# Performance work log

Hardware: AMD Instinct MI355X
Metric: run time of the kernel (lower is better)

Reference implementation:

```python
import jax, jax.numpy as jnp
import numpy as np
import math


def setup_inputs() -> dict:
    key = jax.random.key(0)
    kq, kk, kv = jax.random.split(key, 3)
    B, H, S, D = 8, 12, 4096, 64
    q = jax.random.normal(kq, (B, H, S, D), dtype=jnp.float32)
    k = jax.random.normal(kk, (B, H, S, D), dtype=jnp.float32)
    v = jax.random.normal(kv, (B, H, S, D), dtype=jnp.float32)
    return {"q": q, "k": k, "v": v}


def reference(q, k, v):
    B, H, S, D = q.shape
    topk = int(2 * math.sqrt(S))  # 128 for S=4096
    # importance = mean + std (torch.std is unbiased -> ddof=1)
    importance = q.mean(axis=-1) + jnp.std(q, axis=-1, ddof=1)  # [B,H,S]
    _, idx = jax.lax.top_k(importance, topk)  # [B,H,topk]
    idx_e = idx[..., None]  # [B,H,topk,1]
    q_s = jnp.take_along_axis(q, idx_e, axis=2)  # [B,H,topk,D]
    k_s = jnp.take_along_axis(k, idx_e, axis=2)
    v_s = jnp.take_along_axis(v, idx_e, axis=2)
    scores = jnp.einsum('bhtd,bhsd->bhts', q_s, k_s) / math.sqrt(D)
    attn = jax.nn.softmax(scores, axis=-1)
    out_s = jnp.einsum('bhts,bhsd->bhtd', attn, v_s)  # [B,H,topk,D]
    # scatter back into a full tensor (torch uses empty_like; we use zeros
    # for the unselected positions so the output is deterministic)
    bI = jnp.arange(B)[:, None, None]
    hI = jnp.arange(H)[None, :, None]
    out = jnp.zeros_like(v).at[bI, hI, idx].set(out_s)  # [B,H,S,D]
    Himg = int(math.sqrt(S))
    return out.reshape(B, -1, Himg, Himg)  # [B, H*D, Himg, Himg]
```

## Files before the change

### kernel.cpp

```cpp
#include <hip/hip_runtime.h>
#include <hip/hip_fp16.h>
#include <math.h>

#define BH_N 96
#define S_N 4096
#define D_N 64
#define TOPK 128

typedef unsigned long long ull;

__device__ __forceinline__ ull orderKey(double d) {
  ull u = (ull)__double_as_longlong(d);
  if (u & 0x8000000000000000ULL) u = ~u;
  else u |= 0x8000000000000000ULL;
  return u;
}

__global__ __launch_bounds__(256)
void imp_zero_kernel(const float* __restrict__ q, float* __restrict__ out,
                     ull* __restrict__ keys) {
  const int tid = threadIdx.x;
  const size_t off = (size_t)blockIdx.x * 1024 + (size_t)tid * 4;
  const float4 v = *reinterpret_cast<const float4*>(q + off);
  float4 z; z.x = z.y = z.z = z.w = 0.f;
  *reinterpret_cast<float4*>(out + off) = z;

  double s  = (double)v.x + (double)v.y + (double)v.z + (double)v.w;
  double ss = (double)v.x * v.x + (double)v.y * v.y +
              (double)v.z * v.z + (double)v.w * v.w;
#pragma unroll
  for (int m = 1; m < 16; m <<= 1) {
    s  += __shfl_xor(s, m, 64);
    ss += __shfl_xor(ss, m, 64);
  }
  if ((tid & 15) == 0) {
    double mean = s * (1.0 / 64.0);
    double var = (ss - s * s * (1.0 / 64.0)) * (1.0 / 63.0);
    if (var < 0.0) var = 0.0;
    keys[(size_t)blockIdx.x * 16 + (tid >> 4)] = orderKey(mean + sqrt(var));
  }
}

__global__ __launch_bounds__(1024)
void sel_kernel(const ull* __restrict__ keys, int* __restrict__ idx_out) {
  __shared__ int red[2][16];
  __shared__ int s_idx[TOPK];
  __shared__ int s_tidx[1024];
  __shared__ int s_cnt, s_tcnt;

  const int tid = threadIdx.x;
  const int lane = tid & 63;
  const int wv = tid >> 6;
  const int bh = blockIdx.x;
  const ull* kb = keys + (size_t)bh * S_N;

  ull key[4];
#pragma unroll
  for (int i = 0; i < 4; ++i) key[i] = kb[i * 1024 + tid];

  if (tid == 0) { s_cnt = 0; s_tcnt = 0; }

  ull lo = 0ULL, hi = ~0ULL;
  int p = 0;
  while (lo < hi) {
    ull d = hi - lo;
    ull mid = lo + (d >> 1) + (d & 1ULL);
    int c = 0;
#pragma unroll
    for (int i = 0; i < 4; ++i) c += __popcll(__ballot(key[i] >= mid));
    if (lane == 0) red[p][wv] = c;
    __syncthreads();
    int total = 0;
#pragma unroll
    for (int w = 0; w < 16; ++w) total += red[p][w];
    if (total >= TOPK) lo = mid; else hi = mid - 1;
    p ^= 1;
  }
  const ull T = lo;

#pragma unroll
  for (int i = 0; i < 4; ++i) {
    if (key[i] > T) {
      int slot = atomicAdd(&s_cnt, 1);
      s_idx[slot] = i * 1024 + tid;
    } else if (key[i] == T) {
      int sl = atomicAdd(&s_tcnt, 1);
      if (sl < 1024) s_tidx[sl] = i * 1024 + tid;
    }
  }
  __syncthreads();
  const int nsel = s_cnt;
  const int need = TOPK - nsel;
  if (wv == 0 && need > 0) {
    int t = s_tcnt < 1024 ? s_tcnt : 1024;
    for (int sel = 0; sel < need; ++sel) {
      int mymin = 0x7fffffff;
      for (int j = lane; j < t; j += 64) mymin = min(mymin, s_tidx[j]);
#pragma unroll
      for (int m = 1; m < 64; m <<= 1) mymin = min(mymin, __shfl_xor(mymin, m, 64));
      if (lane == 0) s_idx[nsel + sel] = mymin;
      for (int j = lane; j < t; j += 64)
        if (s_tidx[j] == mymin) s_tidx[j] = 0x7fffffff;
    }
  }
  __syncthreads();
  if (tid < TOPK) idx_out[bh * TOPK + tid] = s_idx[tid];
}

__global__ __launch_bounds__(256)
void attn_kernel(const float* __restrict__ q, const float* __restrict__ k,
                 const float* __restrict__ v, const int* __restrict__ idx_all,
                 float* __restrict__ out) {
  __shared__ __align__(16) float sQ[32 * 65];
  __shared__ __align__(16) float sB[64 * 65];
  __shared__ __align__(16) __half sP[32 * 132];
  __shared__ int s_idx[TOPK];

  const int tid = threadIdx.x;
  const int bh = blockIdx.x >> 2;
  const int sub = blockIdx.x & 3;
  if (tid < TOPK) s_idx[tid] = idx_all[bh * TOPK + tid];

  const size_t base = (size_t)bh * S_N * D_N;
  const int rgrp = tid >> 4;
  const int c4 = (tid & 15) * 4;
  const int rr = tid >> 4;
  const int cc = tid & 15;

  __syncthreads();

#pragma unroll
  for (int it = 0; it < 2; ++it) {
    int r = it * 16 + rgrp;
    int srow = s_idx[sub * 32 + r];
    float4 val = *reinterpret_cast<const float4*>(q + base + (size_t)srow * D_N + c4);
    sQ[r * 65 + c4 + 0] = val.x; sQ[r * 65 + c4 + 1] = val.y;
    sQ[r * 65 + c4 + 2] = val.z; sQ[r * 65 + c4 + 3] = val.w;
  }

  float acc[2][8];
#pragma unroll
  for (int j = 0; j < 2; ++j)
#pragma unroll
    for (int m = 0; m < 8; ++m) acc[j][m] = 0.f;

  for (int h = 0; h < 2; ++h) {
    __syncthreads();
#pragma unroll
    for (int it = 0; it < 4; ++it) {
      int r = it * 16 + rgrp;
      int srow = s_idx[h * 64 + r];
      float4 val = *reinterpret_cast<const float4*>(k + base + (size_t)srow * D_N + c4);
      sB[r * 65 + c4 + 0] = val.x; sB[r * 65 + c4 + 1] = val.y;
      sB[r * 65 + c4 + 2] = val.z; sB[r * 65 + c4 + 3] = val.w;
    }
    __syncthreads();
    for (int kk = 0; kk < 64; kk += 2) {
#pragma unroll
      for (int u = 0; u < 2; ++u) {
        float qv0 = sQ[(2 * rr + 0) * 65 + kk + u];
        float qv1 = sQ[(2 * rr + 1) * 65 + kk + u];
        float kv[4];
#pragma unroll
        for (int m = 0; m < 4; ++m) kv[m] = sB[(cc * 4 + m) * 65 + kk + u];
#pragma unroll
        for (int m = 0; m < 4; ++m) {
          acc[0][h * 4 + m] += qv0 * kv[m];
          acc[1][h * 4 + m] += qv1 * kv[m];
        }
      }
    }
  }

  float rmax[2], rsum[2];
#pragma unroll
  for (int j = 0; j < 2; ++j) {
    float mx = acc[j][0];
#pragma unroll
    for (int m = 1; m < 8; ++m) mx = fmaxf(mx, acc[j][m]);
    rmax[j] = mx;
  }
#pragma unroll
  for (int mm = 1; mm < 16; mm <<= 1)
#pragma unroll
    for (int j = 0; j < 2; ++j) rmax[j] = fmaxf(rmax[j], __shfl_xor(rmax[j], mm, 64));
#pragma unroll
  for (int j = 0; j < 2; ++j) {
    float sum = 0.f;
#pragma unroll
    for (int m = 0; m < 8; ++m) {
      float pe = __expf(0.125f * (acc[j][m] - rmax[j]));
      acc[j][m] = pe;
      sum += pe;
    }
    rsum[j] = sum;
  }
#pragma unroll
  for (int mm = 1; mm < 16; mm <<= 1)
#pragma unroll
    for (int j = 0; j < 2; ++j) rsum[j] += __shfl_xor(rsum[j], mm, 64);
#pragma unroll
  for (int j = 0; j < 2; ++j) {
    float rinv = 1.f / rsum[j];
#pragma unroll
    for (int h2 = 0; h2 < 2; ++h2)
#pragma unroll
      for (int m = 0; m < 4; ++m) {
        int col = h2 * 64 + cc * 4 + m;
        sP[(2 * rr + j) * 132 + col] = __float2half_rn(acc[j][h2 * 4 + m] * rinv);
      }
  }

  float acc2[2][4];
#pragma unroll
  for (int j = 0; j < 2; ++j)
#pragma unroll
    for (int m = 0; m < 4; ++m) acc2[j][m] = 0.f;

  for (int h = 0; h < 2; ++h) {
    __syncthreads();
#pragma unroll
    for (int it = 0; it < 4; ++it) {
      int r = it * 16 + rgrp;
      int srow = s_idx[h * 64 + r];
      float4 val = *reinterpret_cast<const float4*>(v + base + (size_t)srow * D_N + c4);
      sB[r * 65 + c4 + 0] = val.x; sB[r * 65 + c4 + 1] = val.y;
      sB[r * 65 + c4 + 2] = val.z; sB[r * 65 + c4 + 3] = val.w;
    }
    __syncthreads();
    for (int s2 = 0; s2 < 64; ++s2) {
      int scol = h * 64 + s2;
      float pj0 = __half2float(sP[(2 * rr + 0) * 132 + scol]);
      float pj1 = __half2float(sP[(2 * rr + 1) * 132 + scol]);
      float vm[4];
#pragma unroll
      for (int m = 0; m < 4; ++m) vm[m] = sB[s2 * 65 + cc * 4 + m];
#pragma unroll
      for (int m = 0; m < 4; ++m) {
        acc2[0][m] += pj0 * vm[m];
        acc2[1][m] += pj1 * vm[m];
      }
    }
  }

#pragma unroll
  for (int j = 0; j < 2; ++j) {
    int srow = s_idx[sub * 32 + 2 * rr + j];
    float4 val;
    val.x = acc2[j][0]; val.y = acc2[j][1]; val.z = acc2[j][2]; val.w = acc2[j][3];
    *reinterpret_cast<float4*>(out + base + (size_t)srow * D_N + cc * 4) = val;
  }
}

extern "C" void kernel_launch(void* const* d_in, const int* in_sizes, int n_in,
                              void* d_out, int out_size, void* d_ws, size_t ws_size,
                              hipStream_t stream) {
  const float* q = (const float*)d_in[0];
  const float* k = (const float*)d_in[1];
  const float* v = (const float*)d_in[2];
  float* out = (float*)d_out;
  ull* keys = (ull*)d_ws;
  int* idx = (int*)((char*)d_ws + (size_t)BH_N * S_N * 8);

  imp_zero_kernel<<<24576, 256, 0, stream>>>(q, out, keys);
  sel_kernel<<<BH_N, 1024, 0, stream>>>(keys, idx);
  attn_kernel<<<BH_N * 4, 256, 0, stream>>>(q, k, v, idx, out);
}
```

Before: 307.8 us.

## Replace bit-wise binary search top-k threshold with 8-pass radix select

The top-k selection kernel now finds the 128th-largest key with an 8-bit radix select (8 histogram passes) instead of a 64-iteration binary search over the 64-bit key range, which needed a block-wide sync per iteration. Blocks shrink to 256 threads, each holding 16 keys. Ties at the threshold are resolved by a single wave scanning keys in index order with ballots, replacing the serial repeated-min loop. Shared-memory atomics on histograms may contend when keys cluster in a few bins.

Result: no change. 311.3 us (+1.1%).

```diff
diff --git a/kernel.cpp b/kernel.cpp
--- a/kernel.cpp
+++ b/kernel.cpp
@@ -41,12 +41,12 @@
   }
 }
 
-__global__ __launch_bounds__(1024)
+__global__ __launch_bounds__(256)
 void sel_kernel(const ull* __restrict__ keys, int* __restrict__ idx_out) {
-  __shared__ int red[2][16];
+  __shared__ int hist[2][256];
   __shared__ int s_idx[TOPK];
-  __shared__ int s_tidx[1024];
-  __shared__ int s_cnt, s_tcnt;
+  __shared__ int sD, sRem;
+  __shared__ int s_cnt;
 
   const int tid = threadIdx.x;
   const int lane = tid & 63;
@@ -54,53 +54,85 @@
   const int bh = blockIdx.x;
   const ull* kb = keys + (size_t)bh * S_N;
 
-  ull key[4];
-#pragma unroll
-  for (int i = 0; i < 4; ++i) key[i] = kb[i * 1024 + tid];
-
-  if (tid == 0) { s_cnt = 0; s_tcnt = 0; }
-
-  ull lo = 0ULL, hi = ~0ULL;
+  ull key[16];
+#pragma unroll
+  for (int i = 0; i < 16; ++i) key[i] = kb[i * 256 + tid];
+
+  hist[0][tid] = 0;
+  hist[1][tid] = 0;
+  if (tid == 0) { s_cnt = 0; }
+  __syncthreads();
+
+  ull prefix = 0;
+  int rem = TOPK;
   int p = 0;
-  while (lo < hi) {
-    ull d = hi - lo;
-    ull mid = lo + (d >> 1) + (d & 1ULL);
-    int c = 0;
-#pragma unroll
-    for (int i = 0; i < 4; ++i) c += __popcll(__ballot(key[i] >= mid));
-    if (lane == 0) red[p][wv] = c;
-    __syncthreads();
-    int total = 0;
-#pragma unroll
-    for (int w = 0; w < 16; ++w) total += red[p][w];
-    if (total >= TOPK) lo = mid; else hi = mid - 1;
+#pragma unroll 1
+  for (int b = 0; b < 8; ++b) {
+    const int shift = 56 - 8 * b;
+    if (b == 0) {
+#pragma unroll
+      for (int i = 0; i < 16; ++i)
+        atomicAdd(&hist[p][(int)((key[i] >> 56) & 255ULL)], 1);
+    } else {
+#pragma unroll
+      for (int i = 0; i < 16; ++i) {
+        if (((key[i] ^ prefix) >> (shift + 8)) == 0)
+          atomicAdd(&hist[p][(int)((key[i] >> shift) & 255ULL)], 1);
+      }
+    }
+    __syncthreads();
+    if (wv == 0) {
+      int rloc = rem;
+      for (int c = 0; c < 4; ++c) {
+        int d = 255 - (c * 64 + lane);
+        int cnt = hist[p][d];
+        int pre = cnt;
+#pragma unroll
+        for (int m = 1; m < 64; m <<= 1) {
+          int t = __shfl_up(pre, m, 64);
+          if (lane >= m) pre += t;
+        }
+        int tot = __shfl(pre, 63, 64);
+        if (rloc <= tot) {
+          ull mask = __ballot(pre >= rloc);
+          int l = __ffsll((long long)mask) - 1;
+          int preL = __shfl(pre, l, 64);
+          int cntL = __shfl(cnt, l, 64);
+          if (lane == 0) { sD = 255 - (c * 64 + l); sRem = rloc - (preL - cntL); }
+          break;
+        }
+        rloc -= tot;
+      }
+    } else {
+      for (int j = tid - 64; j < 256; j += 192) hist[p ^ 1][j] = 0;
+    }
+    __syncthreads();
+    prefix |= ((ull)sD) << shift;
+    rem = sRem;
     p ^= 1;
   }
-  const ull T = lo;
-
-#pragma unroll
-  for (int i = 0; i < 4; ++i) {
+  const ull T = prefix;
+
+#pragma unroll
+  for (int i = 0; i < 16; ++i) {
     if (key[i] > T) {
       int slot = atomicAdd(&s_cnt, 1);
-      s_idx[slot] = i * 1024 + tid;
-    } else if (key[i] == T) {
-      int sl = atomicAdd(&s_tcnt, 1);
-      if (sl < 1024) s_tidx[sl] = i * 1024 + tid;
+      s_idx[slot] = i * 256 + tid;
     }
   }
   __syncthreads();
   const int nsel = s_cnt;
-  const int need = TOPK - nsel;
-  if (wv == 0 && need > 0) {
-    int t = s_tcnt < 1024 ? s_tcnt : 1024;
-    for (int sel = 0; sel < need; ++sel) {
-      int mymin = 0x7fffffff;
-      for (int j = lane; j < t; j += 64) mymin = min(mymin, s_tidx[j]);
-#pragma unroll
-      for (int m = 1; m < 64; m <<= 1) mymin = min(mymin, __shfl_xor(mymin, m, 64));
-      if (lane == 0) s_idx[nsel + sel] = mymin;
-      for (int j = lane; j < t; j += 64)
-        if (s_tidx[j] == mymin) s_tidx[j] = 0x7fffffff;
+  if (wv == 0) {
+    int running = 0;
+    for (int base = 0; base < S_N && running < rem; base += 64) {
+      ull kk2 = kb[base + lane];
+      ull mask = __ballot(kk2 == T);
+      if (kk2 == T) {
+        int below = __popcll(mask & ((1ULL << lane) - 1ULL));
+        int pos = running + below;
+        if (pos < rem) s_idx[nsel + pos] = base + lane;
+      }
+      running += __popcll(mask);
     }
   }
   __syncthreads();
@@ -263,6 +295,6 @@
   int* idx = (int*)((char*)d_ws + (size_t)BH_N * S_N * 8);
 
   imp_zero_kernel<<<24576, 256, 0, stream>>>(q, out, keys);
-  sel_kernel<<<BH_N, 1024, 0, stream>>>(keys, idx);
+  sel_kernel<<<BH_N, 256, 0, stream>>>(keys, idx);
   attn_kernel<<<BH_N * 4, 256, 0, stream>>>(q, k, v, idx, out);
 }
```
